# Kernel tuning notes

Hardware: AMD Instinct MI355X
Metric: run time of the kernel (lower is better)

## Reference

```python
import jax, jax.numpy as jnp
import numpy as np

H = 4      # num_heads
C = 64     # attention_num_c
C_Z = 128  # num_in_c (pair rep channels)
C_T = 64   # num_in_c_kv (template pair channels)


def setup_inputs() -> dict:
    key = jax.random.key(0)
    ks = jax.random.split(key, 7)
    B, T, R = 1, 4, 384
    z2d = jax.random.normal(ks[0], (B, R, R, C_Z), dtype=jnp.float32)
    t2d = jax.random.normal(ks[1], (B, T, R, R, C_T), dtype=jnp.float32)
    s = 0.02
    Wq = jax.random.normal(ks[2], (C_Z, H * C), dtype=jnp.float32) * s
    Wk = jax.random.normal(ks[3], (C_T, H * C), dtype=jnp.float32) * s
    Wv = jax.random.normal(ks[4], (C_T, H * C), dtype=jnp.float32) * s
    Wo = jax.random.normal(ks[5], (H * C, C_Z), dtype=jnp.float32) * s
    bo = jax.random.normal(ks[6], (C_Z,), dtype=jnp.float32) * s
    return {"z2d": z2d, "t2d": t2d, "Wq": Wq, "Wk": Wk, "Wv": Wv, "Wo": Wo, "bo": bo}


def reference(z2d, t2d, Wq, Wk, Wv, Wo, bo):
    B, R = z2d.shape[0], z2d.shape[-2]
    T = t2d.shape[1]
    P = R * R  # residue-pair axis
    # query: one query per residue pair
    zq = z2d.reshape(B, P, 1, C_Z)
    # templates become the key/value axis per residue pair
    tkv = jnp.transpose(t2d, (0, 2, 3, 1, 4)).reshape(B, P, T, C_T)
    q = (zq @ Wq).reshape(B, P, 1, H, C) * (C ** -0.5)
    k = (tkv @ Wk).reshape(B, P, T, H, C)
    v = (tkv @ Wv).reshape(B, P, T, H, C)
    logits = jnp.einsum('bpqhc,bpkhc->bphqk', q, k)  # [B,P,H,1,T]
    weights = jax.nn.softmax(logits, axis=-1)
    weighted_avg = jnp.einsum('bphqk,bpkhc->bpqhc', weights, v)  # [B,P,1,H,C]
    out = weighted_avg.reshape(B, P, 1, H * C) @ Wo + bo
    return out.reshape(B, R, R, C_Z)
```

## Files before the change

### kernel.cpp

```cpp
#include <hip/hip_runtime.h>


#define R_    384
#define P_    (R_ * R_)
#define PB    32
#define NPB   256
#define NT_   18

typedef __attribute__((ext_vector_type(8))) short  short8;
typedef __attribute__((ext_vector_type(4))) float  f32x4;

union S8U { short8 s8; unsigned u[4]; };

__device__ __forceinline__ unsigned short f2bf(float f) {
  unsigned u = __float_as_uint(f);
  unsigned r = ((u >> 16) & 1u) + 0x7FFFu;
  return (unsigned short)((u + r) >> 16);
}
__device__ __forceinline__ float bf2f(unsigned short s) {
  return __uint_as_float(((unsigned)s) << 16);
}
__device__ __forceinline__ unsigned cvtpk(float lo, float hi) {
  unsigned d;
  asm("v_cvt_pk_bf16_f32 %0, %1, %2" : "=v"(d) : "v"(lo), "v"(hi));
  return d;
}
__device__ __forceinline__ int swz(int p, int c) {
  return p * 256 + ((((c >> 3) ^ (p & 31)) << 3) | (c & 7));
}
#define SB() __builtin_amdgcn_sched_barrier(0)
#define BAR() do { \
    asm volatile("s_waitcnt lgkmcnt(0)\ns_barrier" ::: "memory"); \
    SB(); \
  } while (0)

__device__ __forceinline__ void dma16(const float* g, void* lds) {
  __builtin_amdgcn_global_load_lds((const __attribute__((address_space(1))) unsigned*)g,
                                   (__attribute__((address_space(3))) unsigned*)lds,
                                   16, 0, 0);
}

__global__ void prep_kernel(const float* __restrict__ Wq, const float* __restrict__ Wk,
                            const float* __restrict__ Wv, const float* __restrict__ Wo,
                            unsigned short* __restrict__ AbarT,
                            unsigned short* __restrict__ MbarT) {
  int tid = blockIdx.x * blockDim.x + threadIdx.x;
  if (tid < 256 * 128) {
    int n = tid >> 7, i = tid & 127;
    int h = n >> 6, j = n & 63;
    const float* wq = Wq + i * 256 + h * 64;
    const float* wk = Wk + j * 256 + h * 64;
    float acc = 0.f;
#pragma unroll 8
    for (int c = 0; c < 64; ++c) acc += wq[c] * wk[c];
    AbarT[n * 128 + i] = f2bf(acc * 0.125f);
  } else {
    int t2 = tid - 256 * 128;
    int o = t2 >> 8, k = t2 & 255;
    int h = k >> 6, j = k & 63;
    const float* wv = Wv + j * 256 + h * 64;
    const float* wo = Wo + (h * 64) * 128 + o;
    float acc = 0.f;
#pragma unroll 8
    for (int c = 0; c < 64; ++c) acc += wv[c] * wo[c * 128];
    MbarT[o * 256 + k] = f2bf(acc);
  }
}

__global__ __launch_bounds__(512, 2) void attn_kernel(
    const float* __restrict__ z2d, const float* __restrict__ t2d,
    const unsigned short* __restrict__ AbarT, const unsigned short* __restrict__ MbarT,
    const float* __restrict__ bo, float* __restrict__ out) {
  extern __shared__ char smem[];
  float*          sTf = (float*)smem;
  unsigned short* sG  = (unsigned short*)(smem + 98304);

  const int tid  = threadIdx.x;
  const int wv_  = tid >> 6;
  const int lane = tid & 63;
  const int l = lane & 15;
  const int q = lane >> 4;
  const int mt = wv_ & 1;
  const int ng = wv_ >> 1;

  const int dp  = wv_ * 4 + (lane >> 4);
  const int dcf = (((lane & 15) ^ ((lane >> 4) & 3)) << 2);

  const int ap = tid >> 4, asub = tid & 15;
  const int ah = asub >> 2, au = asub & 3;
  const int aoG0 = swz(ap, ah * 64 + au * 16);
  const int aoG1 = swz(ap, ah * 64 + au * 16 + 8);
  int aoK[4];
#pragma unroll
  for (int j = 0; j < 4; ++j)
    aoK[j] = ap * 64 + ((((au * 4 + j) ^ (ap & 3))) << 2);

  const int p2g = mt * 16 + l;

  short8 ab[4][4];
#pragma unroll
  for (int kk = 0; kk < 4; ++kk)
#pragma unroll
    for (int i = 0; i < 4; ++i) {
      const int n = (ng * 4 + i) * 16 + l;
      ab[kk][i] = *(const short8*)(AbarT + n * 128 + kk * 32 + q * 8);
    }
  short8 mb0[8], mb1[8];
#pragma unroll
  for (int kk = 0; kk < 8; ++kk) {
    mb0[kk] = *(const short8*)(MbarT + (size_t)(ng * 32 + l) * 256 + kk * 32 + q * 8);
    mb1[kk] = *(const short8*)(MbarT + (size_t)(ng * 32 + 16 + l) * 256 + kk * 32 + q * 8);
  }
  const float bo0 = bo[ng * 32 + l];
  const float bo1 = bo[ng * 32 + 16 + l];
  SB();
  {
    const size_t P00 = (size_t)blockIdx.x * PB;
    char* dst0 = (char*)sTf + wv_ * 1024;
#pragma unroll
    for (int m = 0; m < 4; ++m)
      dma16(t2d + ((size_t)m * P_ + P00 + dp) * 64 + dcf, dst0 + m * 8192);
    const size_t P01 = P00 + (size_t)NPB * PB;
    char* dst1 = (char*)sTf + 32768 + wv_ * 1024;
#pragma unroll
    for (int m = 0; m < 4; ++m)
      dma16(t2d + ((size_t)m * P_ + P01 + dp) * 64 + dcf, dst1 + m * 8192);
  }
  SB();
  float4 zb[8];
  {
    const float* zr = z2d + ((size_t)blockIdx.x * PB + mt * 16 + l) * 128;
#pragma unroll
    for (int kk = 0; kk < 4; ++kk) {
      zb[2 * kk]     = *(const float4*)(zr + kk * 32 + q * 8);
      zb[2 * kk + 1] = *(const float4*)(zr + kk * 32 + q * 8 + 4);
    }
  }
  BAR();

#pragma unroll 1
  for (int k = 0; k < NT_; ++k) {
    const int slT = (k % 3);
    const int slG = k & 1;
    const size_t P0  = (size_t)(blockIdx.x + (size_t)k * NPB) * PB;
    const size_t P0n = P0 + (size_t)NPB * PB;

    if (k + 2 < NT_) {
      char* dst = (char*)sTf + ((k + 2) % 3) * 32768 + wv_ * 1024;
      const size_t P02 = P0 + 2 * (size_t)NPB * PB;
#pragma unroll
      for (int m = 0; m < 4; ++m)
        dma16(t2d + ((size_t)m * P_ + P02 + dp) * 64 + dcf, dst + m * 8192);
    }
    SB();
    if (k > 0) {
      const unsigned short* sGp = sG + (slG ^ 1) * 8192;
      f32x4 a20 = f32x4{0.f, 0.f, 0.f, 0.f};
      f32x4 a21 = f32x4{0.f, 0.f, 0.f, 0.f};
#pragma unroll
      for (int kk = 0; kk < 8; ++kk) {
        short8 af2 = *(const short8*)(sGp + p2g * 256 + (((kk * 4 + q) ^ p2g) << 3));
        a20 = __builtin_amdgcn_mfma_f32_16x16x32_bf16(af2, mb0[kk], a20, 0, 0, 0);
        a21 = __builtin_amdgcn_mfma_f32_16x16x32_bf16(af2, mb1[kk], a21, 0, 0, 0);
      }
      const size_t rb = (P0 - (size_t)NPB * PB + (size_t)(mt * 16 + q * 4)) * 128;
#pragma unroll
      for (int r = 0; r < 4; ++r) {
        out[rb + r * 128 + ng * 32 + l]      = a20[r] + bo0;
        out[rb + r * 128 + ng * 32 + 16 + l] = a21[r] + bo1;
      }
    }
    SB();
    {
      f32x4 a1[4];
#pragma unroll
      for (int i = 0; i < 4; ++i) a1[i] = f32x4{0.f, 0.f, 0.f, 0.f};
#pragma unroll
      for (int kk = 0; kk < 4; ++kk) {
        S8U af;
        af.u[0] = cvtpk(zb[2 * kk].x,     zb[2 * kk].y);
        af.u[1] = cvtpk(zb[2 * kk].z,     zb[2 * kk].w);
        af.u[2] = cvtpk(zb[2 * kk + 1].x, zb[2 * kk + 1].y);
        af.u[3] = cvtpk(zb[2 * kk + 1].z, zb[2 * kk + 1].w);
#pragma unroll
        for (int i = 0; i < 4; ++i)
          a1[i] = __builtin_amdgcn_mfma_f32_16x16x32_bf16(af.s8, ab[kk][i], a1[i], 0, 0, 0);
      }
      unsigned short* sGc = sG + slG * 8192;
#pragma unroll
      for (int i = 0; i < 4; ++i) {
        const int c = (ng * 4 + i) * 16 + l;
#pragma unroll
        for (int r = 0; r < 4; ++r)
          sGc[swz(mt * 16 + q * 4 + r, c)] = f2bf(a1[i][r]);
      }
    }
    SB();
    if (k + 1 < NT_) {
      const float* zr = z2d + (P0n + (size_t)(mt * 16 + l)) * 128;
#pragma unroll
      for (int kk = 0; kk < 4; ++kk) {
        zb[2 * kk]     = *(const float4*)(zr + kk * 32 + q * 8);
        zb[2 * kk + 1] = *(const float4*)(zr + kk * 32 + q * 8 + 4);
      }
    }
    SB();
    BAR();

    {
      const float* Kt = sTf + slT * 8192;
      unsigned short* sGc = sG + slG * 8192;
      short8 g0 = *(const short8*)(sGc + aoG0);
      short8 g1 = *(const short8*)(sGc + aoG1);
      float lg0 = 0.f, lg1 = 0.f, lg2 = 0.f, lg3 = 0.f;
#pragma unroll
      for (int j = 0; j < 4; ++j) {
        const float ga = bf2f((unsigned short)((j < 2) ? g0[4 * j]     : g1[4 * (j - 2)]));
        const float gb = bf2f((unsigned short)((j < 2) ? g0[4 * j + 1] : g1[4 * (j - 2) + 1]));
        const float gc = bf2f((unsigned short)((j < 2) ? g0[4 * j + 2] : g1[4 * (j - 2) + 2]));
        const float gd = bf2f((unsigned short)((j < 2) ? g0[4 * j + 3] : g1[4 * (j - 2) + 3]));
        float4 k0 = *(const float4*)(Kt +        aoK[j]);
        float4 k1 = *(const float4*)(Kt + 2048 + aoK[j]);
        float4 k2 = *(const float4*)(Kt + 4096 + aoK[j]);
        float4 k3 = *(const float4*)(Kt + 6144 + aoK[j]);
        lg0 += ga * k0.x + gb * k0.y + gc * k0.z + gd * k0.w;
        lg1 += ga * k1.x + gb * k1.y + gc * k1.z + gd * k1.w;
        lg2 += ga * k2.x + gb * k2.y + gc * k2.z + gd * k2.w;
        lg3 += ga * k3.x + gb * k3.y + gc * k3.z + gd * k3.w;
      }
      lg0 += __shfl_xor(lg0, 1); lg0 += __shfl_xor(lg0, 2);
      lg1 += __shfl_xor(lg1, 1); lg1 += __shfl_xor(lg1, 2);
      lg2 += __shfl_xor(lg2, 1); lg2 += __shfl_xor(lg2, 2);
      lg3 += __shfl_xor(lg3, 1); lg3 += __shfl_xor(lg3, 2);
      const float mx = fmaxf(fmaxf(lg0, lg1), fmaxf(lg2, lg3));
      float e0 = __expf(lg0 - mx), e1 = __expf(lg1 - mx);
      float e2 = __expf(lg2 - mx), e3 = __expf(lg3 - mx);
      const float inv = 1.f / (e0 + e1 + e2 + e3);
      e0 *= inv; e1 *= inv; e2 *= inv; e3 *= inv;
#pragma unroll
      for (int j = 0; j < 4; ++j) {
        float4 k0 = *(const float4*)(Kt +        aoK[j]);
        float4 k1 = *(const float4*)(Kt + 2048 + aoK[j]);
        float4 k2 = *(const float4*)(Kt + 4096 + aoK[j]);
        float4 k3 = *(const float4*)(Kt + 6144 + aoK[j]);
        float s0 = e0 * k0.x + e1 * k1.x + e2 * k2.x + e3 * k3.x;
        float s1 = e0 * k0.y + e1 * k1.y + e2 * k2.y + e3 * k3.y;
        float s2 = e0 * k0.z + e1 * k1.z + e2 * k2.z + e3 * k3.z;
        float s3 = e0 * k0.w + e1 * k1.w + e2 * k2.w + e3 * k3.w;
        uint2 w2; w2.x = cvtpk(s0, s1); w2.y = cvtpk(s2, s3);
        *(uint2*)(sGc + swz(ap, ah * 64 + au * 16 + j * 4)) = w2;
      }
    }
    BAR();
  }

  {
    const unsigned short* sGp = sG + 8192;
    f32x4 a20 = f32x4{0.f, 0.f, 0.f, 0.f};
    f32x4 a21 = f32x4{0.f, 0.f, 0.f, 0.f};
#pragma unroll
    for (int kk = 0; kk < 8; ++kk) {
      short8 af2 = *(const short8*)(sGp + p2g * 256 + (((kk * 4 + q) ^ p2g) << 3));
      a20 = __builtin_amdgcn_mfma_f32_16x16x32_bf16(af2, mb0[kk], a20, 0, 0, 0);
      a21 = __builtin_amdgcn_mfma_f32_16x16x32_bf16(af2, mb1[kk], a21, 0, 0, 0);
    }
    const size_t rb = ((size_t)(blockIdx.x + (size_t)(NT_ - 1) * NPB) * PB
                       + (size_t)(mt * 16 + q * 4)) * 128;
#pragma unroll
    for (int r = 0; r < 4; ++r) {
      out[rb + r * 128 + ng * 32 + l]      = a20[r] + bo0;
      out[rb + r * 128 + ng * 32 + 16 + l] = a21[r] + bo1;
    }
  }
}

extern "C" void kernel_launch(void* const* d_in, const int* in_sizes, int n_in,
                              void* d_out, int out_size, void* d_ws, size_t ws_size,
                              hipStream_t stream) {
  const float* z2d = (const float*)d_in[0];
  const float* t2d = (const float*)d_in[1];
  const float* Wq  = (const float*)d_in[2];
  const float* Wk  = (const float*)d_in[3];
  const float* Wv  = (const float*)d_in[4];
  const float* Wo  = (const float*)d_in[5];
  const float* bo  = (const float*)d_in[6];

  unsigned short* AbarT = (unsigned short*)d_ws;
  unsigned short* MbarT = AbarT + 256 * 128;
  float* out = (float*)d_out;

  static bool attr_set = false;
  if (!attr_set) {
    (void)hipFuncSetAttribute((const void*)attn_kernel,
                              hipFuncAttributeMaxDynamicSharedMemorySize, 131072);
    attr_set = true;
  }

  hipLaunchKernelGGL(prep_kernel, dim3(256), dim3(256), 0, stream,
                     Wq, Wk, Wv, Wo, AbarT, MbarT);
  hipLaunchKernelGGL(attn_kernel, dim3(NPB), dim3(512), 131072, stream,
                     z2d, t2d, AbarT, MbarT, bo, out);
}
```

Before: 308.1 us.

## Halve pair tile to 16, use 256-thread blocks with 4-deep template prefetch

Shrinks each block's residue-pair tile from 32 to 16 and the block from 512 to 256 threads, doubling the grid to 512 blocks. Template loads move to a 4-slot ring with a 3-step prefetch lead issued after the attention step, and the mid-iteration barrier becomes an lgkmcnt wait because each wave now owns its own template slice and G rows. The per-wave mapping is rewritten so one wave handles one template/head group, which changes the shuffle reduction pattern and LDS swizzle. The aim is more blocks in flight, deeper memory latency hiding and fewer block-wide barriers. The cost is more per-block setup, since each block reloads the weight fragments and processes less work per load.

```diff
diff --git a/kernel.cpp b/kernel.cpp
--- a/kernel.cpp
+++ b/kernel.cpp
@@ -3,8 +3,8 @@
 
 #define R_    384
 #define P_    (R_ * R_)
-#define PB    32
-#define NPB   256
+#define PB    16
+#define NPB   512
 #define NT_   18
 
 typedef __attribute__((ext_vector_type(8))) short  short8;
@@ -25,8 +25,8 @@
   asm("v_cvt_pk_bf16_f32 %0, %1, %2" : "=v"(d) : "v"(lo), "v"(hi));
   return d;
 }
-__device__ __forceinline__ int swz(int p, int c) {
-  return p * 256 + ((((c >> 3) ^ (p & 31)) << 3) | (c & 7));
+__device__ __forceinline__ int swz16(int p, int c) {
+  return p * 256 + ((((c >> 3) ^ p) << 3) | (c & 7));
 }
 #define SB() __builtin_amdgcn_sched_barrier(0)
 #define BAR() do { \
@@ -67,103 +67,77 @@
   }
 }
 
-__global__ __launch_bounds__(512, 2) void attn_kernel(
+__global__ __launch_bounds__(256, 2) void attn_kernel(
     const float* __restrict__ z2d, const float* __restrict__ t2d,
     const unsigned short* __restrict__ AbarT, const unsigned short* __restrict__ MbarT,
     const float* __restrict__ bo, float* __restrict__ out) {
   extern __shared__ char smem[];
   float*          sTf = (float*)smem;
-  unsigned short* sG  = (unsigned short*)(smem + 98304);
+  unsigned short* sG  = (unsigned short*)(smem + 65536);
 
   const int tid  = threadIdx.x;
-  const int wv_  = tid >> 6;
+  const int ng   = tid >> 6;
   const int lane = tid & 63;
   const int l = lane & 15;
   const int q = lane >> 4;
-  const int mt = wv_ & 1;
-  const int ng = wv_ >> 1;
-
-  const int dp  = wv_ * 4 + (lane >> 4);
-  const int dcf = (((lane & 15) ^ ((lane >> 4) & 3)) << 2);
-
-  const int ap = tid >> 4, asub = tid & 15;
-  const int ah = asub >> 2, au = asub & 3;
-  const int aoG0 = swz(ap, ah * 64 + au * 16);
-  const int aoG1 = swz(ap, ah * 64 + au * 16 + 8);
-  int aoK[4];
-#pragma unroll
-  for (int j = 0; j < 4; ++j)
-    aoK[j] = ap * 64 + ((((au * 4 + j) ^ (ap & 3))) << 2);
-
-  const int p2g = mt * 16 + l;
 
   short8 ab[4][4];
 #pragma unroll
   for (int kk = 0; kk < 4; ++kk)
 #pragma unroll
-    for (int i = 0; i < 4; ++i) {
-      const int n = (ng * 4 + i) * 16 + l;
-      ab[kk][i] = *(const short8*)(AbarT + n * 128 + kk * 32 + q * 8);
-    }
+    for (int i = 0; i < 4; ++i)
+      ab[kk][i] = *(const short8*)(AbarT + ((ng * 4 + i) * 16 + l) * 128 + kk * 32 + q * 8);
   short8 mb0[8], mb1[8];
 #pragma unroll
   for (int kk = 0; kk < 8; ++kk) {
-    mb0[kk] = *(const short8*)(MbarT + (size_t)(ng * 32 + l) * 256 + kk * 32 + q * 8);
-    mb1[kk] = *(const short8*)(MbarT + (size_t)(ng * 32 + 16 + l) * 256 + kk * 32 + q * 8);
+    mb0[kk] = *(const short8*)(MbarT + (size_t)((ng * 2) * 16 + l) * 256 + kk * 32 + q * 8);
+    mb1[kk] = *(const short8*)(MbarT + (size_t)((ng * 2 + 1) * 16 + l) * 256 + kk * 32 + q * 8);
   }
   const float bo0 = bo[ng * 32 + l];
   const float bo1 = bo[ng * 32 + 16 + l];
   SB();
-  {
-    const size_t P00 = (size_t)blockIdx.x * PB;
-    char* dst0 = (char*)sTf + wv_ * 1024;
-#pragma unroll
-    for (int m = 0; m < 4; ++m)
-      dma16(t2d + ((size_t)m * P_ + P00 + dp) * 64 + dcf, dst0 + m * 8192);
-    const size_t P01 = P00 + (size_t)NPB * PB;
-    char* dst1 = (char*)sTf + 32768 + wv_ * 1024;
-#pragma unroll
-    for (int m = 0; m < 4; ++m)
-      dma16(t2d + ((size_t)m * P_ + P01 + dp) * 64 + dcf, dst1 + m * 8192);
+
+#pragma unroll
+  for (int s = 0; s < 3; ++s) {
+    const size_t P0s = (size_t)(blockIdx.x + s * NPB) * PB;
+    char* dst = (char*)sTf + s * 16384 + ng * 4096;
+#pragma unroll
+    for (int m = 0; m < 4; ++m) {
+      const int dp  = m * 4 + q;
+      const int dcf = (l ^ (((m & 1) << 2) | q)) << 2;
+      dma16(t2d + ((size_t)ng * P_ + P0s + dp) * 64 + dcf, dst + m * 1024);
+    }
   }
   SB();
   float4 zb[8];
   {
-    const float* zr = z2d + ((size_t)blockIdx.x * PB + mt * 16 + l) * 128;
+    const float* zr = z2d + ((size_t)blockIdx.x * PB + l) * 128;
 #pragma unroll
     for (int kk = 0; kk < 4; ++kk) {
       zb[2 * kk]     = *(const float4*)(zr + kk * 32 + q * 8);
       zb[2 * kk + 1] = *(const float4*)(zr + kk * 32 + q * 8 + 4);
     }
   }
+  SB();
+  asm volatile("s_waitcnt vmcnt(8)" ::: "memory");
+  SB();
   BAR();
 
 #pragma unroll 1
   for (int k = 0; k < NT_; ++k) {
-    const int slT = (k % 3);
-    const int slG = k & 1;
-    const size_t P0  = (size_t)(blockIdx.x + (size_t)k * NPB) * PB;
-    const size_t P0n = P0 + (size_t)NPB * PB;
-
-    if (k + 2 < NT_) {
-      char* dst = (char*)sTf + ((k + 2) % 3) * 32768 + wv_ * 1024;
-      const size_t P02 = P0 + 2 * (size_t)NPB * PB;
-#pragma unroll
-      for (int m = 0; m < 4; ++m)
-        dma16(t2d + ((size_t)m * P_ + P02 + dp) * 64 + dcf, dst + m * 8192);
-    }
-    SB();
+    const size_t P0 = (size_t)(blockIdx.x + (size_t)k * NPB) * PB;
+
     if (k > 0) {
-      const unsigned short* sGp = sG + (slG ^ 1) * 8192;
+      const unsigned short* sGp = sG + ((k - 1) & 1) * 4096;
       f32x4 a20 = f32x4{0.f, 0.f, 0.f, 0.f};
       f32x4 a21 = f32x4{0.f, 0.f, 0.f, 0.f};
 #pragma unroll
       for (int kk = 0; kk < 8; ++kk) {
-        short8 af2 = *(const short8*)(sGp + p2g * 256 + (((kk * 4 + q) ^ p2g) << 3));
+        short8 af2 = *(const short8*)(sGp + l * 256 + (((kk * 4 + q) ^ l) << 3));
         a20 = __builtin_amdgcn_mfma_f32_16x16x32_bf16(af2, mb0[kk], a20, 0, 0, 0);
         a21 = __builtin_amdgcn_mfma_f32_16x16x32_bf16(af2, mb1[kk], a21, 0, 0, 0);
       }
-      const size_t rb = (P0 - (size_t)NPB * PB + (size_t)(mt * 16 + q * 4)) * 128;
+      const size_t rb = ((size_t)(blockIdx.x + (size_t)(k - 1) * NPB) * PB + q * 4) * 128;
 #pragma unroll
       for (int r = 0; r < 4; ++r) {
         out[rb + r * 128 + ng * 32 + l]      = a20[r] + bo0;
@@ -186,18 +160,18 @@
         for (int i = 0; i < 4; ++i)
           a1[i] = __builtin_amdgcn_mfma_f32_16x16x32_bf16(af.s8, ab[kk][i], a1[i], 0, 0, 0);
       }
-      unsigned short* sGc = sG + slG * 8192;
+      unsigned short* sGc = sG + (k & 1) * 4096;
 #pragma unroll
       for (int i = 0; i < 4; ++i) {
-        const int c = (ng * 4 + i) * 16 + l;
+        const int c = ng * 64 + i * 16 + l;
 #pragma unroll
         for (int r = 0; r < 4; ++r)
-          sGc[swz(mt * 16 + q * 4 + r, c)] = f2bf(a1[i][r]);
+          sGc[swz16(q * 4 + r, c)] = f2bf(a1[i][r]);
       }
     }
     SB();
     if (k + 1 < NT_) {
-      const float* zr = z2d + (P0n + (size_t)(mt * 16 + l)) * 128;
+      const float* zr = z2d + (P0 + (size_t)NPB * PB + l) * 128;
 #pragma unroll
       for (int kk = 0; kk < 4; ++kk) {
         zb[2 * kk]     = *(const float4*)(zr + kk * 32 + q * 8);
@@ -205,13 +179,17 @@
       }
     }
     SB();
-    BAR();
-
+    asm volatile("s_waitcnt lgkmcnt(0)" ::: "memory");
+    SB();
     {
-      const float* Kt = sTf + slT * 8192;
-      unsigned short* sGc = sG + slG * 8192;
-      short8 g0 = *(const short8*)(sGc + aoG0);
-      short8 g1 = *(const short8*)(sGc + aoG1);
+      const float* Kt = sTf + (k & 3) * 4096;
+      unsigned short* sGc = sG + (k & 1) * 4096;
+      short8 g0 = *(const short8*)(sGc + swz16(l, ng * 64 + q * 16));
+      short8 g1 = *(const short8*)(sGc + swz16(l, ng * 64 + q * 16 + 8));
+      int aoK[4];
+#pragma unroll
+      for (int j = 0; j < 4; ++j)
+        aoK[j] = l * 64 + (((q * 4 + j) ^ (l & 7)) << 2);
       float lg0 = 0.f, lg1 = 0.f, lg2 = 0.f, lg3 = 0.f;
 #pragma unroll
       for (int j = 0; j < 4; ++j) {
@@ -220,52 +198,64 @@
         const float gc = bf2f((unsigned short)((j < 2) ? g0[4 * j + 2] : g1[4 * (j - 2) + 2]));
         const float gd = bf2f((unsigned short)((j < 2) ? g0[4 * j + 3] : g1[4 * (j - 2) + 3]));
         float4 k0 = *(const float4*)(Kt +        aoK[j]);
-        float4 k1 = *(const float4*)(Kt + 2048 + aoK[j]);
-        float4 k2 = *(const float4*)(Kt + 4096 + aoK[j]);
-        float4 k3 = *(const float4*)(Kt + 6144 + aoK[j]);
+        float4 k1 = *(const float4*)(Kt + 1024 + aoK[j]);
+        float4 k2 = *(const float4*)(Kt + 2048 + aoK[j]);
+        float4 k3 = *(const float4*)(Kt + 3072 + aoK[j]);
         lg0 += ga * k0.x + gb * k0.y + gc * k0.z + gd * k0.w;
         lg1 += ga * k1.x + gb * k1.y + gc * k1.z + gd * k1.w;
         lg2 += ga * k2.x + gb * k2.y + gc * k2.z + gd * k2.w;
         lg3 += ga * k3.x + gb * k3.y + gc * k3.z + gd * k3.w;
       }
-      lg0 += __shfl_xor(lg0, 1); lg0 += __shfl_xor(lg0, 2);
-      lg1 += __shfl_xor(lg1, 1); lg1 += __shfl_xor(lg1, 2);
-      lg2 += __shfl_xor(lg2, 1); lg2 += __shfl_xor(lg2, 2);
-      lg3 += __shfl_xor(lg3, 1); lg3 += __shfl_xor(lg3, 2);
+      lg0 += __shfl_xor(lg0, 16); lg0 += __shfl_xor(lg0, 32);
+      lg1 += __shfl_xor(lg1, 16); lg1 += __shfl_xor(lg1, 32);
+      lg2 += __shfl_xor(lg2, 16); lg2 += __shfl_xor(lg2, 32);
+      lg3 += __shfl_xor(lg3, 16); lg3 += __shfl_xor(lg3, 32);
       const float mx = fmaxf(fmaxf(lg0, lg1), fmaxf(lg2, lg3));
       float e0 = __expf(lg0 - mx), e1 = __expf(lg1 - mx);
       float e2 = __expf(lg2 - mx), e3 = __expf(lg3 - mx);
       const float inv = 1.f / (e0 + e1 + e2 + e3);
       e0 *= inv; e1 *= inv; e2 *= inv; e3 *= inv;
+      asm volatile("" ::: "memory");
 #pragma unroll
       for (int j = 0; j < 4; ++j) {
         float4 k0 = *(const float4*)(Kt +        aoK[j]);
-        float4 k1 = *(const float4*)(Kt + 2048 + aoK[j]);
-        float4 k2 = *(const float4*)(Kt + 4096 + aoK[j]);
-        float4 k3 = *(const float4*)(Kt + 6144 + aoK[j]);
+        float4 k1 = *(const float4*)(Kt + 1024 + aoK[j]);
+        float4 k2 = *(const float4*)(Kt + 2048 + aoK[j]);
+        float4 k3 = *(const float4*)(Kt + 3072 + aoK[j]);
         float s0 = e0 * k0.x + e1 * k1.x + e2 * k2.x + e3 * k3.x;
         float s1 = e0 * k0.y + e1 * k1.y + e2 * k2.y + e3 * k3.y;
         float s2 = e0 * k0.z + e1 * k1.z + e2 * k2.z + e3 * k3.z;
         float s3 = e0 * k0.w + e1 * k1.w + e2 * k2.w + e3 * k3.w;
         uint2 w2; w2.x = cvtpk(s0, s1); w2.y = cvtpk(s2, s3);
-        *(uint2*)(sGc + swz(ap, ah * 64 + au * 16 + j * 4)) = w2;
-      }
-    }
+        *(uint2*)(sGc + swz16(l, ng * 64 + q * 16 + 4 * j)) = w2;
+      }
+    }
+    SB();
+    if (k + 3 < NT_) {
+      const size_t P03 = P0 + 3 * (size_t)NPB * PB;
+      char* dst = (char*)sTf + ((k + 3) & 3) * 16384 + ng * 4096;
+#pragma unroll
+      for (int m = 0; m < 4; ++m) {
+        const int dp  = m * 4 + q;
+        const int dcf = (l ^ (((m & 1) << 2) | q)) << 2;
+        dma16(t2d + ((size_t)ng * P_ + P03 + dp) * 64 + dcf, dst + m * 1024);
+      }
+    }
+    SB();
     BAR();
   }
 
   {
-    const unsigned short* sGp = sG + 8192;
+    const unsigned short* sGp = sG + ((NT_ - 1) & 1) * 4096;
     f32x4 a20 = f32x4{0.f, 0.f, 0.f, 0.f};
     f32x4 a21 = f32x4{0.f, 0.f, 0.f, 0.f};
 #pragma unroll
     for (int kk = 0; kk < 8; ++kk) {
-      short8 af2 = *(const short8*)(sGp + p2g * 256 + (((kk * 4 + q) ^ p2g) << 3));
+      short8 af2 = *(const short8*)(sGp + l * 256 + (((kk * 4 + q) ^ l) << 3));
       a20 = __builtin_amdgcn_mfma_f32_16x16x32_bf16(af2, mb0[kk], a20, 0, 0, 0);
       a21 = __builtin_amdgcn_mfma_f32_16x16x32_bf16(af2, mb1[kk], a21, 0, 0, 0);
     }
-    const size_t rb = ((size_t)(blockIdx.x + (size_t)(NT_ - 1) * NPB) * PB
-                       + (size_t)(mt * 16 + q * 4)) * 128;
+    const size_t rb = ((size_t)(blockIdx.x + (size_t)(NT_ - 1) * NPB) * PB + q * 4) * 128;
 #pragma unroll
     for (int r = 0; r < 4; ++r) {
       out[rb + r * 128 + ng * 32 + l]      = a20[r] + bo0;
@@ -292,12 +282,12 @@
   static bool attr_set = false;
   if (!attr_set) {
     (void)hipFuncSetAttribute((const void*)attn_kernel,
-                              hipFuncAttributeMaxDynamicSharedMemorySize, 131072);
+                              hipFuncAttributeMaxDynamicSharedMemorySize, 81920);
     attr_set = true;
   }
 
   hipLaunchKernelGGL(prep_kernel, dim3(256), dim3(256), 0, stream,
                      Wq, Wk, Wv, Wo, AbarT, MbarT);
-  hipLaunchKernelGGL(attn_kernel, dim3(NPB), dim3(512), 131072, stream,
+  hipLaunchKernelGGL(attn_kernel, dim3(NPB), dim3(256), 81920, stream,
                      z2d, t2d, AbarT, MbarT, bo, out);
 }
```

Measured after the change: 304.7 us. Within noise of the previous version (-1.1%).
